# Performance work log

Hardware: AMD Instinct MI355X
Metric: run time of the kernel (lower is better)

Reference implementation:

```python
import jax, jax.numpy as jnp
import numpy as np

# ---------- constants ----------
EPS = 1e-5
_rng = np.random.default_rng(0)
_P = _rng.normal(size=(8, 3))
_P /= np.linalg.norm(_P, axis=1, keepdims=True)

def _y2_np(p):
    x, y, z = p[:, 0], p[:, 1], p[:, 2]
    return np.stack([x * y, y * z, 3 * z * z - 1, x * z, x * x - y * y], axis=-1)

_A2 = np.linalg.pinv(_y2_np(_P)).astype(np.float32)  # [5,8]
P_C = jnp.asarray(_P.astype(np.float32))
A2_C = jnp.asarray(_A2)
NORM_CONST = np.float32(1.0 / np.sqrt(20.0))  # avg_num_neighbors ** -0.5
# res update (buffer zeros, not learnable): sigmoid(0)=0.5
_U = 0.5
C_OLD = np.float32(1.0 / np.sqrt(_U * _U + 1.0))
C_NEW = np.float32(_U * C_OLD)


def _y2(p):  # real l=2 monomial basis on unit vectors
    x, y, z = p[..., 0], p[..., 1], p[..., 2]
    return jnp.stack([x * y, y * z, 3.0 * z * z - 1.0, x * z, x * x - y * y], axis=-1)


def _frame(v):  # [E,3] -> R [E,3,3] with R @ v_hat = z
    n = v / jnp.linalg.norm(v, axis=-1, keepdims=True)
    z = jnp.array([0.0, 0.0, 1.0], v.dtype)
    xa = jnp.array([1.0, 0.0, 0.0], v.dtype)
    a = jnp.where(jnp.abs(n[:, 2:3]) < 0.99, z, xa)
    e1 = jnp.cross(a, n)
    e1 = e1 / jnp.linalg.norm(e1, axis=-1, keepdims=True)
    e2 = jnp.cross(n, e1)
    return jnp.stack([e1, e2, n], axis=1)


def _wigner_d2(R):  # [E,3,3] -> D2 [E,5,5] via sample-point fit
    pts = jnp.einsum('pj,eij->epi', P_C, R)  # R @ p_k, [E,8,3]
    M = _y2(pts)  # [E,8,5] = Y_P @ D^T
    Dt = jnp.einsum('ap,epb->eab', A2_C, M)  # [E,5,5]
    return jnp.swapaxes(Dt, 1, 2)


def _sln(x, w0, b0, w1, w2):  # separable equivariant layernorm, 32x0e+16x1e+8x2e
    s = x[:, :32]
    v1 = x[:, 32:80].reshape(-1, 16, 3)
    v2 = x[:, 80:120].reshape(-1, 8, 5)
    mu = jnp.mean(s, axis=-1, keepdims=True)
    var = jnp.mean((s - mu) ** 2, axis=-1, keepdims=True)
    s = (s - mu) * jax.lax.rsqrt(var + EPS) * w0 + b0
    var1 = jnp.mean(v1 ** 2, axis=(1, 2))  # degree-balanced component variance
    var2 = jnp.mean(v2 ** 2, axis=(1, 2))
    inv = jax.lax.rsqrt(0.5 * (var1 + var2) + EPS)[:, None, None]
    v1 = v1 * inv * w1[None, :, None]
    v2 = v2 * inv * w2[None, :, None]
    return jnp.concatenate([s, v1.reshape(-1, 48), v2.reshape(-1, 40)], axis=-1)


def _ir_linear(x, W0, b0, W1, W2):  # irreps-wise linear 32x0e+16x1e+8x2e -> same
    s = x[:, :32] @ (W0 / np.sqrt(32.0)) + b0
    v1 = jnp.einsum('eui,uv->evi', x[:, 32:80].reshape(-1, 16, 3), W1) / np.sqrt(16.0)
    v2 = jnp.einsum('eui,uv->evi', x[:, 80:120].reshape(-1, 8, 5), W2) / np.sqrt(8.0)
    return jnp.concatenate([s, v1.reshape(-1, 48), v2.reshape(-1, 40)], axis=-1)


def _so2(x_cat, R, D2f, D2b, w):  # SO2 linear with per-edge dynamic weights
    E = x_cat.shape[0]
    w0 = w[:, :8960].reshape(E, 112, 80)
    w1r = w[:, 8960:10112].reshape(E, 48, 24)
    w1i = w[:, 10112:11264].reshape(E, 48, 24)
    w2r = w[:, 11264:11392].reshape(E, 16, 8)
    w2i = w[:, 11392:11520].reshape(E, 16, 8)
    # split concatenated [in + hidden] blocks
    s = jnp.concatenate([x_cat[:, :32], x_cat[:, 120:152]], axis=-1)  # [E,64]
    v1 = jnp.concatenate([x_cat[:, 32:80].reshape(E, 16, 3),
                          x_cat[:, 152:200].reshape(E, 16, 3)], axis=1)  # [E,32,3]
    v2 = jnp.concatenate([x_cat[:, 80:120].reshape(E, 8, 5),
                          x_cat[:, 200:240].reshape(E, 16 // 2, 5)], axis=1)  # [E,16,5]
    # rotate into edge-aligned frame
    v1 = jnp.einsum('eij,euj->eui', R, v1)
    v2 = jnp.einsum('eij,euj->eui', D2f, v2)
    in0 = jnp.concatenate([s, v1[:, :, 1], v2[:, :, 2]], axis=-1)   # m=0, [E,112]
    inn1 = jnp.concatenate([v1[:, :, 0], v2[:, :, 1]], axis=-1)     # m=-1, [E,48]
    inp1 = jnp.concatenate([v1[:, :, 2], v2[:, :, 3]], axis=-1)     # m=+1
    inn2 = v2[:, :, 0]  # m=-2
    inp2 = v2[:, :, 4]  # m=+2
    out0 = jnp.einsum('ei,eio->eo', in0, w0) / np.sqrt(112.0)
    op1 = (jnp.einsum('ei,eio->eo', inp1, w1r) - jnp.einsum('ei,eio->eo', inn1, w1i)) / np.sqrt(48.0)
    on1 = (jnp.einsum('ei,eio->eo', inn1, w1r) + jnp.einsum('ei,eio->eo', inp1, w1i)) / np.sqrt(48.0)
    op2 = (jnp.einsum('ei,eio->eo', inp2, w2r) - jnp.einsum('ei,eio->eo', inn2, w2i)) / np.sqrt(16.0)
    on2 = (jnp.einsum('ei,eio->eo', inn2, w2r) + jnp.einsum('ei,eio->eo', inp2, w2i)) / np.sqrt(16.0)
    s_out = out0[:, :56]
    y1 = jnp.stack([on1[:, :16], out0[:, 56:72], op1[:, :16]], axis=-1)  # [E,16,3]
    y2o = jnp.stack([on2, on1[:, 16:24], out0[:, 72:80], op1[:, 16:24], op2], axis=-1)  # [E,8,5]
    # rotate back
    y1 = jnp.einsum('eij,euj->eui', jnp.swapaxes(R, 1, 2), y1)
    y2o = jnp.einsum('eij,euj->eui', D2b, y2o)
    return jnp.concatenate([s_out, y1.reshape(E, 48), y2o.reshape(E, 40)], axis=-1)  # [E,144]


def _gate(m):  # 32x0e scalars | 24x0e gates | 16x1e+8x2e gated
    s = jax.nn.silu(m[:, :32])
    g = jax.nn.sigmoid(m[:, 32:56])
    v1 = m[:, 56:104].reshape(-1, 16, 3) * g[:, :16, None]
    v2 = m[:, 104:144].reshape(-1, 8, 5) * g[:, 16:24, None]
    return jnp.concatenate([s, v1.reshape(-1, 48), v2.reshape(-1, 40)], axis=-1)


def _env(m, we):  # E3ElementLinear: per-mul elementwise weights
    s = m[:, :32] * we[:, :32]
    v1 = m[:, 32:80].reshape(-1, 16, 3) * we[:, 32:48, None]
    v2 = m[:, 80:120].reshape(-1, 8, 5) * we[:, 48:56, None]
    return jnp.concatenate([s, v1.reshape(-1, 48), v2.reshape(-1, 40)], axis=-1)


def setup_inputs() -> dict:
    key = jax.random.key(0)
    ks = jax.random.split(key, 16)
    N, E, L = 512, 10240, 128
    inp = {
        'latents': jax.random.normal(ks[0], (E, L), jnp.float32),
        'node_features': jax.random.normal(ks[1], (N, 120), jnp.float32),
        'hidden_features': jax.random.normal(ks[2], (E, 120), jnp.float32),
        'node_onehot': jnp.ones((N, 16), jnp.float32),
        'edge_vector': jax.random.normal(ks[3], (E, 3), jnp.float32),
        'W_tp': jax.random.normal(ks[4], (L, 11520), jnp.float32),
        'W_env': jax.random.normal(ks[5], (L, 56), jnp.float32),
        'sln_w0': jnp.ones((32,), jnp.float32),
        'sln_b0': jnp.zeros((32,), jnp.float32),
        'sln_w1': jnp.ones((16,), jnp.float32),
        'sln_w2': jnp.ones((8,), jnp.float32),
        'Wp0': jax.random.normal(ks[6], (32, 32), jnp.float32),
        'bp0': jnp.zeros((32,), jnp.float32),
        'Wp1': jax.random.normal(ks[7], (16, 16), jnp.float32),
        'Wp2': jax.random.normal(ks[8], (8, 8), jnp.float32),
        'Wr0': jax.random.normal(ks[9], (32, 32), jnp.float32),
        'br0': jnp.zeros((32,), jnp.float32),
        'Wr1': jax.random.normal(ks[10], (16, 16), jnp.float32),
        'Wr2': jax.random.normal(ks[11], (8, 8), jnp.float32),
        'atom_type': jax.random.randint(ks[12], (N,), 0, 10, jnp.int32),
        'edge_index': jax.random.randint(ks[13], (2, E), 0, N, jnp.int32),
        'active_edges': jnp.arange(E, dtype=jnp.int32),
    }
    return inp


def reference(latents, node_features, hidden_features, node_onehot, edge_vector,
              W_tp, W_env, sln_w0, sln_b0, sln_w1, sln_w2,
              Wp0, bp0, Wp1, Wp2, Wr0, br0, Wr1, Wr2,
              atom_type, edge_index, active_edges):
    n_nodes = node_features.shape[0]
    center = edge_index[0][active_edges]
    nf = _sln(node_features, sln_w0, sln_b0, sln_w1, sln_w2)
    x_cat = jnp.concatenate([nf[center], hidden_features], axis=-1)  # [E,240]
    v = edge_vector[active_edges]
    R = _frame(v)
    D2f = _wigner_d2(R)
    D2b = _wigner_d2(jnp.swapaxes(R, 1, 2))
    wdyn = latents @ (W_tp / np.sqrt(128.0))  # per-edge dynamic SO2 weights
    msg = _so2(x_cat, R, D2f, D2b, wdyn)
    msg = _gate(msg)
    msg = _ir_linear(msg, Wp0, bp0, Wp1, Wp2)
    wenv = latents[active_edges] @ (W_env / np.sqrt(128.0))
    weighted = _env(msg, wenv)
    new_nf = jax.ops.segment_sum(weighted, center, num_segments=n_nodes)
    new_nf = new_nf * NORM_CONST
    res = _ir_linear(node_features, Wr0, br0, Wr1, Wr2)
    return C_NEW * new_nf + C_OLD * res
```

## Files before the change

kernel.cpp:

```cpp
#include <hip/hip_runtime.h>
#include <math.h>

#define E_TOT   10240
#define N_NODES 512
#define NCOL    11520

typedef unsigned short ushort_t;
typedef unsigned int   uint_t;
typedef __bf16 bf16x8 __attribute__((ext_vector_type(8)));
typedef float  f32x4  __attribute__((ext_vector_type(4)));

constexpr float EPSF        = 1e-5f;
constexpr float INV_SQRT128 = 0.08838834764831845f;
constexpr float INV_SQRT112 = 0.09449111825230681f;
constexpr float INV_SQRT48  = 0.14433756729740643f;
constexpr float INV_SQRT32  = 0.17677669529663687f;
constexpr float INV_SQRT16  = 0.25f;
constexpr float INV_SQRT8   = 0.35355339059327373f;
constexpr float SC0 = INV_SQRT128 * INV_SQRT112;
constexpr float SC1 = INV_SQRT128 * INV_SQRT48;
constexpr float SC2 = INV_SQRT128 * INV_SQRT16;
constexpr float C_OLD_ = 0.8944271909999159f;
constexpr float C_NEW_ = 0.4472135954999579f;
constexpr float NORMC  = 0.22360679774997896f;

__device__ __forceinline__ ushort_t f2bf(float x) {
  uint_t u = __float_as_uint(x);
  u = (u + 0x7fffu + ((u >> 16) & 1u)) >> 16;
  return (ushort_t)u;
}

__device__ __forceinline__ void wigner5(const float q[9], float D[25]) {
  const float q0x=q[0],q0y=q[1],q0z=q[2];
  const float q1x=q[3],q1y=q[4],q1z=q[5];
  const float q2x=q[6],q2y=q[7],q2z=q[8];
  D[0]  = q0x*q1y + q1x*q0y;
  D[1]  = q0y*q1z + q1y*q0z;
  D[2]  = 0.5f*(q0z*q1z);
  D[3]  = q0x*q1z + q1x*q0z;
  D[4]  = 0.5f*(q0x*q1x - q0y*q1y);
  D[5]  = q1x*q2y + q2x*q1y;
  D[6]  = q1y*q2z + q2y*q1z;
  D[7]  = 0.5f*(q1z*q2z);
  D[8]  = q1x*q2z + q2x*q1z;
  D[9]  = 0.5f*(q1x*q2x - q1y*q2y);
  D[10] = 6.f*q2x*q2y;
  D[11] = 6.f*q2y*q2z;
  D[12] = 0.5f*(3.f*q2z*q2z - 1.f);
  D[13] = 6.f*q2x*q2z;
  D[14] = 1.5f*(q2x*q2x - q2y*q2y);
  D[15] = q0x*q2y + q2x*q0y;
  D[16] = q0y*q2z + q2y*q0z;
  D[17] = 0.5f*(q0z*q2z);
  D[18] = q0x*q2z + q2x*q0z;
  D[19] = 0.5f*(q0x*q2x - q0y*q2y);
  D[20] = 2.f*(q0x*q0y - q1x*q1y);
  D[21] = 2.f*(q0y*q0z - q1y*q1z);
  D[22] = 0.5f*(q0z*q0z - q1z*q1z);
  D[23] = 2.f*(q0x*q0z - q1x*q1z);
  D[24] = 0.5f*((q0x*q0x - q1x*q1x) - (q0y*q0y - q1y*q1y));
}

__global__ void kA(const float* __restrict__ Wtp, const float* __restrict__ lat,
                   const float* __restrict__ Wenv,
                   ushort_t* __restrict__ Wp,
                   ushort_t* __restrict__ lath, ushort_t* __restrict__ latl,
                   float* __restrict__ oa_g, float* __restrict__ accg,
                   float* __restrict__ WenvT) {
  __shared__ float Wl[128*17];
  const int bid = blockIdx.x;
  const int t = threadIdx.x;
  if (bid < 720) {
    const int nt = bid;
    int col, tt;
    if (nt < 560)      { col = nt/112; tt = nt - col*112; }
    else if (nt < 608) { col = 5;  tt = nt-560; }
    else if (nt < 632) { col = 6;  tt = nt-608; }
    else if (nt < 680) { col = 7;  tt = nt-632; }
    else if (nt < 704) { col = 8;  tt = nt-680; }
    else if (nt < 712) { col = 9;  tt = nt-704; }
    else               { col = 10; tt = nt-712; }
    float sc;
    {
      const int m1 = t & 15, lp = t >> 4;
      int c;
      switch (col) {
        case 5:  c = 8960  + tt*24 + m1;                        sc = SC1; break;
        case 6:  c = 8960  + (2*tt + (m1>>3))*24 + 16 + (m1&7); sc = SC1; break;
        case 7:  c = 10112 + tt*24 + m1;                        sc = SC1; break;
        case 8:  c = 10112 + (2*tt + (m1>>3))*24 + 16 + (m1&7); sc = SC1; break;
        case 9:  c = 11264 + (2*tt + (m1>>3))*8 + (m1&7);       sc = SC2; break;
        case 10: c = 11392 + (2*tt + (m1>>3))*8 + (m1&7);       sc = SC2; break;
        default: c = tt*80 + col*16 + m1;                       sc = SC0; break;
      }
#pragma unroll
      for (int p = 0; p < 8; ++p) {
        int l = p*16 + lp;
        Wl[l*17 + m1] = Wtp[(size_t)l*NCOL + c] * sc;
      }
    }
    __syncthreads();
    const int kc = t >> 6, lane = t & 63;
    const int m = lane & 15, kg = lane >> 4;
    ushort_t hi[8], lo[8];
#pragma unroll
    for (int jj = 0; jj < 8; ++jj) {
      int l = kc*32 + kg*8 + jj;
      float w = Wl[l*17 + m];
      ushort_t h = f2bf(w);
      float hf = __uint_as_float(((uint_t)h) << 16);
      hi[jj] = h;
      lo[jj] = f2bf(w - hf);
    }
    size_t base = ((size_t)nt*8 + kc*2)*512 + (size_t)lane*8;
    *(uint4*)&Wp[base]       = *(const uint4*)hi;
    *(uint4*)&Wp[base + 512] = *(const uint4*)lo;
    return;
  }
  const int j = bid - 720;
  const int idx = j*256 + t;
  {
    float x = lat[idx];
    ushort_t h = f2bf(x);
    float hf = __uint_as_float(((uint_t)h) << 16);
    lath[idx] = h;
    latl[idx] = f2bf(x - hf);
  }
#pragma unroll
  for (int i = t; i < 288; i += 256) oa_g[(size_t)j*288 + i] = 0.f;
  if (j < 240) accg[j*256 + t] = 0.f;
  if (j >= 4000 && j < 4028) {
    int q = (j-4000)*256 + t;
    int o = q >> 7, l = q & 127;
    WenvT[o*128 + l] = Wenv[l*56 + o];
  }
}

__global__ __launch_bounds__(256)
void k2_edge_prep(const float* __restrict__ ndf,
                  const float* __restrict__ hid,
                  const float* __restrict__ evec,
                  const int*   __restrict__ eidx,
                  const int*   __restrict__ act,
                  const float* __restrict__ w0, const float* __restrict__ b0,
                  const float* __restrict__ w1, const float* __restrict__ w2,
                  float* __restrict__ invT,
                  float* __restrict__ Rm,
                  float* __restrict__ D2bm) {
  __shared__ float xs[32][240];
  __shared__ float Rs[32][9];
  __shared__ float Dfs[32][25];
  __shared__ float muS[32], isS[32], invS[32];
  __shared__ int   ctrs[32];
  const int t = threadIdx.x;
  const int e0 = blockIdx.x*32;
  if (t < 32) {
    const int e = e0 + t;
    const int ae = act[e];
    ctrs[t] = eidx[ae];
    float vx = evec[ae*3+0], vy = evec[ae*3+1], vz = evec[ae*3+2];
    float rn = rsqrtf(vx*vx + vy*vy + vz*vz);
    float nx = vx*rn, ny = vy*rn, nz = vz*rn;
    float e1x, e1y, e1z;
    if (fabsf(nz) < 0.99f) { e1x = -ny; e1y = nx;  e1z = 0.f; }
    else                   { e1x = 0.f; e1y = -nz; e1z = ny;  }
    float rl = rsqrtf(e1x*e1x + e1y*e1y + e1z*e1z);
    e1x *= rl; e1y *= rl; e1z *= rl;
    float e2x = ny*e1z - nz*e1y;
    float e2y = nz*e1x - nx*e1z;
    float e2z = nx*e1y - ny*e1x;
    float R[9] = {e1x,e1y,e1z, e2x,e2y,e2z, nx,ny,nz};
#pragma unroll
    for (int jj = 0; jj < 9; ++jj) { Rs[t][jj] = R[jj]; Rm[(size_t)e*9 + jj] = R[jj]; }
    float Df[25];
    wigner5(R, Df);
#pragma unroll
    for (int jj = 0; jj < 25; ++jj) Dfs[t][jj] = Df[jj];
    float Rt[9] = {R[0],R[3],R[6], R[1],R[4],R[7], R[2],R[5],R[8]};
    float Db[25];
    wigner5(Rt, Db);
#pragma unroll
    for (int jj = 0; jj < 25; ++jj) D2bm[(size_t)e*25 + jj] = Db[jj];
  }
  __syncthreads();
  for (int i = t; i < 32*120; i += 256) {
    int s = i/120, jj = i - s*120;
    xs[s][jj]     = ndf[(size_t)ctrs[s]*120 + jj];
    xs[s][120+jj] = hid[(size_t)(e0+s)*120 + jj];
  }
  __syncthreads();
  if (t < 32) {
    float sum = 0.f, sq = 0.f;
#pragma unroll
    for (int i = 0; i < 32; ++i) { float v = xs[t][i]; sum += v; sq += v*v; }
    float mu = sum*(1.f/32.f);
    float var = sq*(1.f/32.f) - mu*mu;
    float v1s = 0.f, v2s = 0.f;
#pragma unroll
    for (int i = 32; i < 80; ++i) { float v = xs[t][i]; v1s += v*v; }
#pragma unroll
    for (int i = 80; i < 120; ++i) { float v = xs[t][i]; v2s += v*v; }
    muS[t] = mu;
    isS[t] = rsqrtf(var + EPSF);
    invS[t] = rsqrtf(0.5f*(v1s*(1.f/48.f) + v2s*(1.f/40.f)) + EPSF);
  }
  __syncthreads();
  const int e = t & 31, rb = t >> 5;
  const float* X  = xs[e];
  const float* Rr = Rs[e];
  const float* Df = Dfs[e];
  const float mu = muS[e], istd = isS[e], inv = invS[e];
#pragma unroll
  for (int r = rb; r < 240; r += 8) {
    float val;
    if (r < 64) {
      if (r < 32) val = (X[r] - mu)*istd*w0[r] + b0[r];
      else        val = X[88 + r];
    } else if (r < 96) {
      int u = r - 64; int b; float fac;
      if (u < 16) { b = 32 + 3*u; fac = inv*w1[u]; } else { b = 152 + 3*(u-16); fac = 1.f; }
      val = (Rr[3]*X[b] + Rr[4]*X[b+1] + Rr[5]*X[b+2])*fac;
    } else if (r < 112) {
      int u = r - 96; int b; float fac;
      if (u < 8) { b = 80 + 5*u; fac = inv*w2[u]; } else { b = 200 + 5*(u-8); fac = 1.f; }
      val = (Df[10]*X[b] + Df[11]*X[b+1] + Df[12]*X[b+2] + Df[13]*X[b+3] + Df[14]*X[b+4])*fac;
    } else if (r < 160) {
      int u = r - 112;
      if (u < 32) {
        int b; float fac;
        if (u < 16) { b = 32 + 3*u; fac = inv*w1[u]; } else { b = 152 + 3*(u-16); fac = 1.f; }
        val = (Rr[0]*X[b] + Rr[1]*X[b+1] + Rr[2]*X[b+2])*fac;
      } else {
        int u2 = u - 32; int b; float fac;
        if (u2 < 8) { b = 80 + 5*u2; fac = inv*w2[u2]; } else { b = 200 + 5*(u2-8); fac = 1.f; }
        val = (Df[5]*X[b] + Df[6]*X[b+1] + Df[7]*X[b+2] + Df[8]*X[b+3] + Df[9]*X[b+4])*fac;
      }
    } else if (r < 208) {
      int u = r - 160;
      if (u < 32) {
        int b; float fac;
        if (u < 16) { b = 32 + 3*u; fac = inv*w1[u]; } else { b = 152 + 3*(u-16); fac = 1.f; }
        val = (Rr[6]*X[b] + Rr[7]*X[b+1] + Rr[8]*X[b+2])*fac;
      } else {
        int u2 = u - 32; int b; float fac;
        if (u2 < 8) { b = 80 + 5*u2; fac = inv*w2[u2]; } else { b = 200 + 5*(u2-8); fac = 1.f; }
        val = (Df[15]*X[b] + Df[16]*X[b+1] + Df[17]*X[b+2] + Df[18]*X[b+3] + Df[19]*X[b+4])*fac;
      }
    } else if (r < 224) {
      int u = r - 208; int b; float fac;
      if (u < 8) { b = 80 + 5*u; fac = inv*w2[u]; } else { b = 200 + 5*(u-8); fac = 1.f; }
      val = (Df[0]*X[b] + Df[1]*X[b+1] + Df[2]*X[b+2] + Df[3]*X[b+3] + Df[4]*X[b+4])*fac;
    } else {
      int u = r - 224; int b; float fac;
      if (u < 8) { b = 80 + 5*u; fac = inv*w2[u]; } else { b = 200 + 5*(u-8); fac = 1.f; }
      val = (Df[20]*X[b] + Df[21]*X[b+1] + Df[22]*X[b+2] + Df[23]*X[b+3] + Df[24]*X[b+4])*fac;
    }
    invT[(size_t)r*E_TOT + e0 + e] = val;
  }
}

__global__ __launch_bounds__(256, 2)
void k3_gemm(const ushort_t* __restrict__ Wp,
             const ushort_t* __restrict__ lath,
             const ushort_t* __restrict__ latl,
             const float*  __restrict__ invT,
             float* __restrict__ oa_g) {
  __shared__ __align__(16) ushort_t abuf[2][8192];
  const int t = threadIdx.x;
  const int wave = t >> 6, lane = t & 63;
  const int le = lane & 15, g = lane >> 4, gh = g >> 1;
  const int fbase = blockIdx.y * 40;
  const int e0w = blockIdx.x*128 + wave*32;
  bf16x8 Bh[4][2], Bl[4][2];
#pragma unroll
  for (int kc = 0; kc < 4; ++kc)
#pragma unroll
    for (int n = 0; n < 2; ++n) {
      size_t off = (size_t)(e0w + n*16 + le)*128 + kc*32 + g*8;
      Bh[kc][n] = *(const bf16x8*)(lath + off);
      Bl[kc][n] = *(const bf16x8*)(latl + off);
    }
  int col, tt;
  if (fbase < 560)      { col = fbase/112; tt = fbase - col*112; }
  else if (fbase < 608) { col = 5;  tt = fbase-560; }
  else if (fbase < 632) { col = 6;  tt = fbase-608; }
  else if (fbase < 680) { col = 7;  tt = fbase-632; }
  else if (fbase < 704) { col = 8;  tt = fbase-680; }
  else if (fbase < 712) { col = 9;  tt = fbase-704; }
  else                  { col = 10; tt = fbase-712; }
  int mP_, mN_, sP_, sN_, segLen; float sg_; bool PAIR_, TWO_;
  auto setParams = [&](int cf) {
    if (cf < 5)       { segLen=112; mP_=0;   mN_=0;   sP_=cf*16; sN_=0;   sg_=1.f;  PAIR_=false; TWO_=false; }
    else if (cf == 5) { segLen=48;  mP_=160; mN_=112; sP_=80;  sN_=104; sg_=1.f;  PAIR_=false; TWO_=true; }
    else if (cf == 6) { segLen=24;  mP_=160; mN_=112; sP_=96;  sN_=120; sg_=1.f;  PAIR_=true;  TWO_=true; }
    else if (cf == 7) { segLen=48;  mP_=112; mN_=160; sP_=80;  sN_=104; sg_=-1.f; PAIR_=false; TWO_=true; }
    else if (cf == 8) { segLen=24;  mP_=112; mN_=160; sP_=96;  sN_=120; sg_=-1.f; PAIR_=true;  TWO_=true; }
    else if (cf == 9) { segLen=8;   mP_=224; mN_=208; sP_=128; sN_=136; sg_=1.f;  PAIR_=true;  TWO_=true; }
    else              { segLen=8;   mP_=208; mN_=224; sP_=128; sN_=136; sg_=-1.f; PAIR_=true;  TWO_=true; }
  };
  setParams(col);
  f32x4 aP0={0,0,0,0}, aP1={0,0,0,0}, aN0={0,0,0,0}, aN1={0,0,0,0};
  auto flush = [&]() {
#pragma unroll
    for (int r = 0; r < 4; ++r) {
      int mm = g*4 + r;
      int sp = sP_ + (PAIR_ ? (mm & 7) : mm);
      atomicAdd(&oa_g[(size_t)(e0w + le)*144 + sp], sg_*aP0[r]);
      atomicAdd(&oa_g[(size_t)(e0w + 16 + le)*144 + sp], sg_*aP1[r]);
      if (TWO_) {
        int sn = sN_ + (PAIR_ ? (mm & 7) : mm);
        atomicAdd(&oa_g[(size_t)(e0w + le)*144 + sn], aN0[r]);
        atomicAdd(&oa_g[(size_t)(e0w + 16 + le)*144 + sn], aN1[r]);
      }
    }
    aP0 = (f32x4){0,0,0,0}; aP1 = (f32x4){0,0,0,0};
    aN0 = (f32x4){0,0,0,0}; aN1 = (f32x4){0,0,0,0};
  };
#pragma unroll
  for (int qq = 0; qq < 4; ++qq) {
    uint4 v = *(const uint4*)(Wp + ((size_t)fbase*8 + wave*4 + qq)*512 + lane*8);
    *(uint4*)&abuf[0][(wave*4 + qq)*512 + lane*8] = v;
  }
  __syncthreads();
  for (int c = 0; c < 20; ++c) {
    const int cb = c & 1, nb = cb ^ 1;
    uint4 pre[4];
    const bool more = (c + 1) < 20;
    if (more) {
#pragma unroll
      for (int qq = 0; qq < 4; ++qq)
        pre[qq] = *(const uint4*)(Wp + ((size_t)(fbase + 2*(c+1))*8 + wave*4 + qq)*512 + lane*8);
    }
#pragma unroll
    for (int lt = 0; lt < 2; ++lt) {
      int idx = PAIR_ ? (2*tt + gh) : tt;
      int rowP = mP_ + idx;
      float mP0 = invT[(size_t)rowP*E_TOT + e0w + le];
      float mP1 = invT[(size_t)rowP*E_TOT + e0w + 16 + le];
      float mN0 = 0.f, mN1 = 0.f;
      if (TWO_) {
        int rowN = mN_ + idx;
        mN0 = invT[(size_t)rowN*E_TOT + e0w + le];
        mN1 = invT[(size_t)rowN*E_TOT + e0w + 16 + le];
      }
      f32x4 d0 = {0,0,0,0}, d1 = {0,0,0,0};
#pragma unroll
      for (int kc = 0; kc < 4; ++kc) {
        bf16x8 Ah = *(const bf16x8*)&abuf[cb][(lt*8 + kc*2 + 0)*512 + lane*8];
        bf16x8 Al = *(const bf16x8*)&abuf[cb][(lt*8 + kc*2 + 1)*512 + lane*8];
        d0 = __builtin_amdgcn_mfma_f32_16x16x32_bf16(Ah, Bh[kc][0], d0, 0, 0, 0);
        d1 = __builtin_amdgcn_mfma_f32_16x16x32_bf16(Ah, Bh[kc][1], d1, 0, 0, 0);
        d0 = __builtin_amdgcn_mfma_f32_16x16x32_bf16(Ah, Bl[kc][0], d0, 0, 0, 0);
        d1 = __builtin_amdgcn_mfma_f32_16x16x32_bf16(Ah, Bl[kc][1], d1, 0, 0, 0);
        d0 = __builtin_amdgcn_mfma_f32_16x16x32_bf16(Al, Bh[kc][0], d0, 0, 0, 0);
        d1 = __builtin_amdgcn_mfma_f32_16x16x32_bf16(Al, Bh[kc][1], d1, 0, 0, 0);
      }
#pragma unroll
      for (int r = 0; r < 4; ++r) { aP0[r] += mP0*d0[r]; aP1[r] += mP1*d1[r]; }
      if (TWO_) {
#pragma unroll
        for (int r = 0; r < 4; ++r) { aN0[r] += mN0*d0[r]; aN1[r] += mN1*d1[r]; }
      }
      tt++;
      if (tt == segLen) { flush(); col++; tt = 0; setParams(col); }
    }
    if (more) {
#pragma unroll
      for (int qq = 0; qq < 4; ++qq)
        *(uint4*)&abuf[nb][(wave*4 + qq)*512 + lane*8] = pre[qq];
    }
    __syncthreads();
  }
  if (tt > 0) flush();
}

__global__ __launch_bounds__(256)
void k4_epi(const float* __restrict__ oa_g, const float* __restrict__ Rm,
            const float* __restrict__ D2bm,
            const float* __restrict__ lat, const float* __restrict__ WenvT,
            const int* __restrict__ eidx, const int* __restrict__ act,
            const float* __restrict__ Wp0, const float* __restrict__ bp0,
            const float* __restrict__ Wp1, const float* __restrict__ Wp2,
            float* __restrict__ accg) {
  __shared__ float sc[4][200];
  const int wave = threadIdx.x >> 6, lane = threadIdx.x & 63;
  const int eg = blockIdx.x*4 + wave;
  const int ae = act[eg];
  const float* o_ = oa_g + (size_t)eg*144;
  if (lane < 56) {
    const float4* wv = (const float4*)(WenvT + lane*128);
    const float4* lv = (const float4*)(lat + (size_t)ae*128);
    float4 s4 = {0,0,0,0};
#pragma unroll
    for (int l4 = 0; l4 < 32; ++l4) {
      float4 a = lv[l4], b = wv[l4];
      s4.x += a.x*b.x; s4.y += a.y*b.y; s4.z += a.z*b.z; s4.w += a.w*b.w;
    }
    sc[wave][144 + lane] = (s4.x + s4.y + s4.z + s4.w) * INV_SQRT128;
    float v = o_[lane];
    sc[wave][lane] = (lane < 32) ? v/(1.f + expf(-v)) : 1.f/(1.f + expf(-v));
  }
  __syncthreads();
  const float* Rr = Rm + (size_t)eg*9;
  const float* Db = D2bm + (size_t)eg*25;
  if (lane < 48) {
    int u = lane/3, cc = lane - u*3;
    float yx = o_[104+u], yy = o_[56+u], yz = o_[80+u];
    float p = Rr[cc]*yx + Rr[3+cc]*yy + Rr[6+cc]*yz;
    sc[wave][56+lane] = p * sc[wave][32+u];
  }
  __syncthreads();
  if (lane < 40) {
    int u = lane/5, ii = lane - u*5;
    float y0 = o_[136+u], y1v = o_[120+u], y2v = o_[72+u], y3 = o_[96+u], y4 = o_[128+u];
    float p = Db[ii*5+0]*y0 + Db[ii*5+1]*y1v + Db[ii*5+2]*y2v + Db[ii*5+3]*y3 + Db[ii*5+4]*y4;
    sc[wave][104+lane] = p * sc[wave][48+u];
  }
  __syncthreads();
  const int ctr = eidx[ae];
  float* dst = accg + (size_t)ctr*120;
  const float* we = &sc[wave][144];
#pragma unroll
  for (int rnd = 0; rnd < 2; ++rnd) {
    int jo = rnd*64 + lane;
    if (jo < 120) {
      float val;
      if (jo < 32) {
        float s = 0.f;
#pragma unroll
        for (int i2 = 0; i2 < 32; ++i2) s += sc[wave][i2]*Wp0[i2*32 + jo];
        val = (s*INV_SQRT32 + bp0[jo]) * we[jo];
      } else if (jo < 80) {
        int jj = jo-32, v = jj/3, cc = jj - v*3;
        float s = 0.f;
#pragma unroll
        for (int u = 0; u < 16; ++u) s += sc[wave][56 + u*3 + cc]*Wp1[u*16 + v];
        val = s*INV_SQRT16*we[32+v];
      } else {
        int jj = jo-80, v = jj/5, ii = jj - v*5;
        float s = 0.f;
#pragma unroll
        for (int u = 0; u < 8; ++u) s += sc[wave][104 + u*5 + ii]*Wp2[u*8 + v];
        val = s*INV_SQRT8*we[48+v];
      }
      atomicAdd(&dst[jo], val);
    }
  }
}

__global__ void k5_final(const float* __restrict__ x_all,
                         const float* __restrict__ Wr0, const float* __restrict__ br0,
                         const float* __restrict__ Wr1, const float* __restrict__ Wr2,
                         const float* __restrict__ accg,
                         float* __restrict__ out) {
  const int n = blockIdx.x;
  const int t = threadIdx.x;
  if (t >= 120) return;
  const float* x = x_all + n*120;
  float r;
  if (t < 32) {
    float s = 0.f;
#pragma unroll
    for (int i = 0; i < 32; ++i) s += x[i]*Wr0[i*32 + t];
    r = s*INV_SQRT32 + br0[t];
  } else if (t < 80) {
    int j = t - 32, v = j/3, cp = j - 3*v;
    float s = 0.f;
#pragma unroll
    for (int u = 0; u < 16; ++u) s += x[32 + u*3 + cp]*Wr1[u*16 + v];
    r = s*INV_SQRT16;
  } else {
    int j = t - 80, v = j/5, cp = j - 5*v;
    float s = 0.f;
#pragma unroll
    for (int u = 0; u < 8; ++u) s += x[80 + u*5 + cp]*Wr2[u*8 + v];
    r = s*INV_SQRT8;
  }
  out[n*120 + t] = C_NEW_*(NORMC*accg[n*120 + t]) + C_OLD_*r;
}

extern "C" void kernel_launch(void* const* d_in, const int* in_sizes, int n_in,
                              void* d_out, int out_size, void* d_ws, size_t ws_size,
                              hipStream_t stream) {
  const float* lat  = (const float*)d_in[0];
  const float* ndf  = (const float*)d_in[1];
  const float* hid  = (const float*)d_in[2];
  const float* evec = (const float*)d_in[4];
  const float* Wtp  = (const float*)d_in[5];
  const float* Wenv = (const float*)d_in[6];
  const float* w0   = (const float*)d_in[7];
  const float* b0   = (const float*)d_in[8];
  const float* w1   = (const float*)d_in[9];
  const float* w2   = (const float*)d_in[10];
  const float* Wp0  = (const float*)d_in[11];
  const float* bp0  = (const float*)d_in[12];
  const float* Wp1  = (const float*)d_in[13];
  const float* Wp2  = (const float*)d_in[14];
  const float* Wr0  = (const float*)d_in[15];
  const float* br0  = (const float*)d_in[16];
  const float* Wr1  = (const float*)d_in[17];
  const float* Wr2  = (const float*)d_in[18];
  const int*   eidx = (const int*)d_in[20];
  const int*   act  = (const int*)d_in[21];
  float* out = (float*)d_out;

  char* p = (char*)d_ws;
  float*    invT  = (float*)(p + 245760);
  float*    Rm    = (float*)(p + 10076160);
  float*    D2bm  = (float*)(p + 10444800);
  float*    accg  = (float*)(p + 13762560);
  float*    oa_g  = (float*)(p + 14008320);
  ushort_t* lath  = (ushort_t*)(p + 19906560);
  ushort_t* latl  = (ushort_t*)(p + 22528000);
  ushort_t* Wpack = (ushort_t*)(p + 25149440);
  float*    WenvT = (float*)(p + 31047680);

  kA<<<5840, 256, 0, stream>>>(Wtp, lat, Wenv, Wpack, lath, latl, oa_g, accg, WenvT);
  k2_edge_prep<<<E_TOT/32, 256, 0, stream>>>(ndf, hid, evec, eidx, act,
                                             w0, b0, w1, w2, invT, Rm, D2bm);
  k3_gemm<<<dim3(E_TOT/128, 18), 256, 0, stream>>>(Wpack, lath, latl, invT, oa_g);
  k4_epi<<<E_TOT/4, 256, 0, stream>>>(oa_g, Rm, D2bm, lat, WenvT, eidx, act,
                                      Wp0, bp0, Wp1, Wp2, accg);
  k5_final<<<N_NODES, 128, 0, stream>>>(ndf, Wr0, br0, Wr1, Wr2, accg, out);
}
```

Before: 324.6 us.

## Fuse prep kernels, scatter directly into output, double GEMM tile per block

Result: faster. 303.3 us (-6.5%).

```diff
diff --git a/kernel.cpp b/kernel.cpp
--- a/kernel.cpp
+++ b/kernel.cpp
@@ -23,6 +23,7 @@
 constexpr float C_OLD_ = 0.8944271909999159f;
 constexpr float C_NEW_ = 0.4472135954999579f;
 constexpr float NORMC  = 0.22360679774997896f;
+constexpr float OUTSC  = C_NEW_ * NORMC;
 
 __device__ __forceinline__ ushort_t f2bf(float x) {
   uint_t u = __float_as_uint(x);
@@ -61,16 +62,26 @@
   D[24] = 0.5f*((q0x*q0x - q1x*q1x) - (q0y*q0y - q1y*q1y));
 }
 
-__global__ void kA(const float* __restrict__ Wtp, const float* __restrict__ lat,
-                   const float* __restrict__ Wenv,
-                   ushort_t* __restrict__ Wp,
-                   ushort_t* __restrict__ lath, ushort_t* __restrict__ latl,
-                   float* __restrict__ oa_g, float* __restrict__ accg,
-                   float* __restrict__ WenvT) {
-  __shared__ float Wl[128*17];
+__global__ __launch_bounds__(256)
+void kAB(const float* __restrict__ Wtp, const float* __restrict__ lat,
+         const float* __restrict__ Wenv,
+         const float* __restrict__ ndf, const float* __restrict__ hid,
+         const float* __restrict__ evec,
+         const int* __restrict__ eidx, const int* __restrict__ act,
+         const float* __restrict__ w0, const float* __restrict__ b0,
+         const float* __restrict__ w1, const float* __restrict__ w2,
+         const float* __restrict__ Wr0, const float* __restrict__ br0,
+         const float* __restrict__ Wr1, const float* __restrict__ Wr2,
+         ushort_t* __restrict__ Wp,
+         ushort_t* __restrict__ lath, ushort_t* __restrict__ latl,
+         float* __restrict__ oa_g, float* __restrict__ WenvT,
+         float* __restrict__ invT, float* __restrict__ Rm,
+         float* __restrict__ D2bm, float* __restrict__ out) {
+  __shared__ __align__(16) char smem[35584];
   const int bid = blockIdx.x;
   const int t = threadIdx.x;
   if (bid < 720) {
+    float* Wl = (float*)smem;
     const int nt = bid;
     int col, tt;
     if (nt < 560)      { col = nt/112; tt = nt - col*112; }
@@ -80,10 +91,9 @@
     else if (nt < 704) { col = 8;  tt = nt-680; }
     else if (nt < 712) { col = 9;  tt = nt-704; }
     else               { col = 10; tt = nt-712; }
-    float sc;
     {
       const int m1 = t & 15, lp = t >> 4;
-      int c;
+      int c; float sc;
       switch (col) {
         case 5:  c = 8960  + tt*24 + m1;                        sc = SC1; break;
         case 6:  c = 8960  + (2*tt + (m1>>3))*24 + 16 + (m1&7); sc = SC1; break;
@@ -117,146 +127,179 @@
     *(uint4*)&Wp[base + 512] = *(const uint4*)lo;
     return;
   }
-  const int j = bid - 720;
-  const int idx = j*256 + t;
-  {
+  if (bid < 5840) {
+    const int j = bid - 720;
+    const int idx = j*256 + t;
     float x = lat[idx];
     ushort_t h = f2bf(x);
     float hf = __uint_as_float(((uint_t)h) << 16);
     lath[idx] = h;
     latl[idx] = f2bf(x - hf);
-  }
-#pragma unroll
-  for (int i = t; i < 288; i += 256) oa_g[(size_t)j*288 + i] = 0.f;
-  if (j < 240) accg[j*256 + t] = 0.f;
-  if (j >= 4000 && j < 4028) {
-    int q = (j-4000)*256 + t;
-    int o = q >> 7, l = q & 127;
-    WenvT[o*128 + l] = Wenv[l*56 + o];
-  }
-}
-
-__global__ __launch_bounds__(256)
-void k2_edge_prep(const float* __restrict__ ndf,
-                  const float* __restrict__ hid,
-                  const float* __restrict__ evec,
-                  const int*   __restrict__ eidx,
-                  const int*   __restrict__ act,
-                  const float* __restrict__ w0, const float* __restrict__ b0,
-                  const float* __restrict__ w1, const float* __restrict__ w2,
-                  float* __restrict__ invT,
-                  float* __restrict__ Rm,
-                  float* __restrict__ D2bm) {
-  __shared__ float xs[32][240];
-  __shared__ float Rs[32][9];
-  __shared__ float Dfs[32][25];
-  __shared__ float muS[32], isS[32], invS[32];
-  __shared__ int   ctrs[32];
-  const int t = threadIdx.x;
-  const int e0 = blockIdx.x*32;
-  if (t < 32) {
-    const int e = e0 + t;
-    const int ae = act[e];
-    ctrs[t] = eidx[ae];
-    float vx = evec[ae*3+0], vy = evec[ae*3+1], vz = evec[ae*3+2];
-    float rn = rsqrtf(vx*vx + vy*vy + vz*vz);
-    float nx = vx*rn, ny = vy*rn, nz = vz*rn;
-    float e1x, e1y, e1z;
-    if (fabsf(nz) < 0.99f) { e1x = -ny; e1y = nx;  e1z = 0.f; }
-    else                   { e1x = 0.f; e1y = -nz; e1z = ny;  }
-    float rl = rsqrtf(e1x*e1x + e1y*e1y + e1z*e1z);
-    e1x *= rl; e1y *= rl; e1z *= rl;
-    float e2x = ny*e1z - nz*e1y;
-    float e2y = nz*e1x - nx*e1z;
-    float e2z = nx*e1y - ny*e1x;
-    float R[9] = {e1x,e1y,e1z, e2x,e2y,e2z, nx,ny,nz};
-#pragma unroll
-    for (int jj = 0; jj < 9; ++jj) { Rs[t][jj] = R[jj]; Rm[(size_t)e*9 + jj] = R[jj]; }
-    float Df[25];
-    wigner5(R, Df);
-#pragma unroll
-    for (int jj = 0; jj < 25; ++jj) Dfs[t][jj] = Df[jj];
-    float Rt[9] = {R[0],R[3],R[6], R[1],R[4],R[7], R[2],R[5],R[8]};
-    float Db[25];
-    wigner5(Rt, Db);
-#pragma unroll
-    for (int jj = 0; jj < 25; ++jj) D2bm[(size_t)e*25 + jj] = Db[jj];
-  }
-  __syncthreads();
-  for (int i = t; i < 32*120; i += 256) {
-    int s = i/120, jj = i - s*120;
-    xs[s][jj]     = ndf[(size_t)ctrs[s]*120 + jj];
-    xs[s][120+jj] = hid[(size_t)(e0+s)*120 + jj];
-  }
-  __syncthreads();
-  if (t < 32) {
-    float sum = 0.f, sq = 0.f;
-#pragma unroll
-    for (int i = 0; i < 32; ++i) { float v = xs[t][i]; sum += v; sq += v*v; }
-    float mu = sum*(1.f/32.f);
-    float var = sq*(1.f/32.f) - mu*mu;
-    float v1s = 0.f, v2s = 0.f;
-#pragma unroll
-    for (int i = 32; i < 80; ++i) { float v = xs[t][i]; v1s += v*v; }
-#pragma unroll
-    for (int i = 80; i < 120; ++i) { float v = xs[t][i]; v2s += v*v; }
-    muS[t] = mu;
-    isS[t] = rsqrtf(var + EPSF);
-    invS[t] = rsqrtf(0.5f*(v1s*(1.f/48.f) + v2s*(1.f/40.f)) + EPSF);
-  }
-  __syncthreads();
-  const int e = t & 31, rb = t >> 5;
-  const float* X  = xs[e];
-  const float* Rr = Rs[e];
-  const float* Df = Dfs[e];
-  const float mu = muS[e], istd = isS[e], inv = invS[e];
-#pragma unroll
-  for (int r = rb; r < 240; r += 8) {
-    float val;
-    if (r < 64) {
-      if (r < 32) val = (X[r] - mu)*istd*w0[r] + b0[r];
-      else        val = X[88 + r];
-    } else if (r < 96) {
-      int u = r - 64; int b; float fac;
-      if (u < 16) { b = 32 + 3*u; fac = inv*w1[u]; } else { b = 152 + 3*(u-16); fac = 1.f; }
-      val = (Rr[3]*X[b] + Rr[4]*X[b+1] + Rr[5]*X[b+2])*fac;
-    } else if (r < 112) {
-      int u = r - 96; int b; float fac;
-      if (u < 8) { b = 80 + 5*u; fac = inv*w2[u]; } else { b = 200 + 5*(u-8); fac = 1.f; }
-      val = (Df[10]*X[b] + Df[11]*X[b+1] + Df[12]*X[b+2] + Df[13]*X[b+3] + Df[14]*X[b+4])*fac;
-    } else if (r < 160) {
-      int u = r - 112;
-      if (u < 32) {
-        int b; float fac;
+#pragma unroll
+    for (int i = t; i < 288; i += 256) oa_g[(size_t)j*288 + i] = 0.f;
+    if (j >= 4000 && j < 4028) {
+      int q = (j-4000)*256 + t;
+      int o = q >> 7, l = q & 127;
+      WenvT[o*128 + l] = Wenv[l*56 + o];
+    }
+    return;
+  }
+  if (bid < 6160) {
+    float (*xs)[240] = (float(*)[240])smem;
+    float (*Rs)[9]   = (float(*)[9])(smem + 30720);
+    float (*Dfs)[25] = (float(*)[25])(smem + 31872);
+    float* muS  = (float*)(smem + 35072);
+    float* isS  = (float*)(smem + 35200);
+    float* invS = (float*)(smem + 35328);
+    int*   ctrs = (int*)(smem + 35456);
+    const int e0 = (bid - 5840)*32;
+    if (t < 32) {
+      const int e = e0 + t;
+      const int ae = act[e];
+      ctrs[t] = eidx[ae];
+      float vx = evec[ae*3+0], vy = evec[ae*3+1], vz = evec[ae*3+2];
+      float rn = rsqrtf(vx*vx + vy*vy + vz*vz);
+      float nx = vx*rn, ny = vy*rn, nz = vz*rn;
+      float e1x, e1y, e1z;
+      if (fabsf(nz) < 0.99f) { e1x = -ny; e1y = nx;  e1z = 0.f; }
+      else                   { e1x = 0.f; e1y = -nz; e1z = ny;  }
+      float rl = rsqrtf(e1x*e1x + e1y*e1y + e1z*e1z);
+      e1x *= rl; e1y *= rl; e1z *= rl;
+      float e2x = ny*e1z - nz*e1y;
+      float e2y = nz*e1x - nx*e1z;
+      float e2z = nx*e1y - ny*e1x;
+      float R[9] = {e1x,e1y,e1z, e2x,e2y,e2z, nx,ny,nz};
+#pragma unroll
+      for (int jj = 0; jj < 9; ++jj) { Rs[t][jj] = R[jj]; Rm[(size_t)e*9 + jj] = R[jj]; }
+      float Df[25];
+      wigner5(R, Df);
+#pragma unroll
+      for (int jj = 0; jj < 25; ++jj) Dfs[t][jj] = Df[jj];
+      float Rt[9] = {R[0],R[3],R[6], R[1],R[4],R[7], R[2],R[5],R[8]};
+      float Db[25];
+      wigner5(Rt, Db);
+#pragma unroll
+      for (int jj = 0; jj < 25; ++jj) D2bm[(size_t)e*25 + jj] = Db[jj];
+    }
+    __syncthreads();
+    for (int i = t; i < 32*120; i += 256) {
+      int s = i/120, jj = i - s*120;
+      xs[s][jj]     = ndf[(size_t)ctrs[s]*120 + jj];
+      xs[s][120+jj] = hid[(size_t)(e0+s)*120 + jj];
+    }
+    __syncthreads();
+    if (t < 32) {
+      float sum = 0.f, sq = 0.f;
+#pragma unroll
+      for (int i = 0; i < 32; ++i) { float v = xs[t][i]; sum += v; sq += v*v; }
+      float mu = sum*(1.f/32.f);
+      float var = sq*(1.f/32.f) - mu*mu;
+      float v1s = 0.f, v2s = 0.f;
+#pragma unroll
+      for (int i = 32; i < 80; ++i) { float v = xs[t][i]; v1s += v*v; }
+#pragma unroll
+      for (int i = 80; i < 120; ++i) { float v = xs[t][i]; v2s += v*v; }
+      muS[t] = mu;
+      isS[t] = rsqrtf(var + EPSF);
+      invS[t] = rsqrtf(0.5f*(v1s*(1.f/48.f) + v2s*(1.f/40.f)) + EPSF);
+    }
+    __syncthreads();
+    const int e = t & 31, rb = t >> 5;
+    const float* X  = xs[e];
+    const float* Rr = Rs[e];
+    const float* Df = Dfs[e];
+    const float mu = muS[e], istd = isS[e], inv = invS[e];
+#pragma unroll
+    for (int r = rb; r < 240; r += 8) {
+      float val;
+      if (r < 64) {
+        if (r < 32) val = (X[r] - mu)*istd*w0[r] + b0[r];
+        else        val = X[88 + r];
+      } else if (r < 96) {
+        int u = r - 64; int b; float fac;
         if (u < 16) { b = 32 + 3*u; fac = inv*w1[u]; } else { b = 152 + 3*(u-16); fac = 1.f; }
-        val = (Rr[0]*X[b] + Rr[1]*X[b+1] + Rr[2]*X[b+2])*fac;
+        val = (Rr[3]*X[b] + Rr[4]*X[b+1] + Rr[5]*X[b+2])*fac;
+      } else if (r < 112) {
+        int u = r - 96; int b; float fac;
+        if (u < 8) { b = 80 + 5*u; fac = inv*w2[u]; } else { b = 200 + 5*(u-8); fac = 1.f; }
+        val = (Df[10]*X[b] + Df[11]*X[b+1] + Df[12]*X[b+2] + Df[13]*X[b+3] + Df[14]*X[b+4])*fac;
+      } else if (r < 160) {
+        int u = r - 112;
+        if (u < 32) {
+          int b; float fac;
+          if (u < 16) { b = 32 + 3*u; fac = inv*w1[u]; } else { b = 152 + 3*(u-16); fac = 1.f; }
+          val = (Rr[0]*X[b] + Rr[1]*X[b+1] + Rr[2]*X[b+2])*fac;
+        } else {
+          int u2 = u - 32; int b; float fac;
+          if (u2 < 8) { b = 80 + 5*u2; fac = inv*w2[u2]; } else { b = 200 + 5*(u2-8); fac = 1.f; }
+          val = (Df[5]*X[b] + Df[6]*X[b+1] + Df[7]*X[b+2] + Df[8]*X[b+3] + Df[9]*X[b+4])*fac;
+        }
+      } else if (r < 208) {
+        int u = r - 160;
+        if (u < 32) {
+          int b; float fac;
+          if (u < 16) { b = 32 + 3*u; fac = inv*w1[u]; } else { b = 152 + 3*(u-16); fac = 1.f; }
+          val = (Rr[6]*X[b] + Rr[7]*X[b+1] + Rr[8]*X[b+2])*fac;
+        } else {
+          int u2 = u - 32; int b; float fac;
+          if (u2 < 8) { b = 80 + 5*u2; fac = inv*w2[u2]; } else { b = 200 + 5*(u2-8); fac = 1.f; }
+          val = (Df[15]*X[b] + Df[16]*X[b+1] + Df[17]*X[b+2] + Df[18]*X[b+3] + Df[19]*X[b+4])*fac;
+        }
+      } else if (r < 224) {
+        int u = r - 208; int b; float fac;
+        if (u < 8) { b = 80 + 5*u; fac = inv*w2[u]; } else { b = 200 + 5*(u-8); fac = 1.f; }
+        val = (Df[0]*X[b] + Df[1]*X[b+1] + Df[2]*X[b+2] + Df[3]*X[b+3] + Df[4]*X[b+4])*fac;
       } else {
-        int u2 = u - 32; int b; float fac;
-        if (u2 < 8) { b = 80 + 5*u2; fac = inv*w2[u2]; } else { b = 200 + 5*(u2-8); fac = 1.f; }
-        val = (Df[5]*X[b] + Df[6]*X[b+1] + Df[7]*X[b+2] + Df[8]*X[b+3] + Df[9]*X[b+4])*fac;
-      }
-    } else if (r < 208) {
-      int u = r - 160;
-      if (u < 32) {
-        int b; float fac;
-        if (u < 16) { b = 32 + 3*u; fac = inv*w1[u]; } else { b = 152 + 3*(u-16); fac = 1.f; }
-        val = (Rr[6]*X[b] + Rr[7]*X[b+1] + Rr[8]*X[b+2])*fac;
-      } else {
-        int u2 = u - 32; int b; float fac;
-        if (u2 < 8) { b = 80 + 5*u2; fac = inv*w2[u2]; } else { b = 200 + 5*(u2-8); fac = 1.f; }
-        val = (Df[15]*X[b] + Df[16]*X[b+1] + Df[17]*X[b+2] + Df[18]*X[b+3] + Df[19]*X[b+4])*fac;
-      }
-    } else if (r < 224) {
-      int u = r - 208; int b; float fac;
-      if (u < 8) { b = 80 + 5*u; fac = inv*w2[u]; } else { b = 200 + 5*(u-8); fac = 1.f; }
-      val = (Df[0]*X[b] + Df[1]*X[b+1] + Df[2]*X[b+2] + Df[3]*X[b+3] + Df[4]*X[b+4])*fac;
+        int u = r - 224; int b; float fac;
+        if (u < 8) { b = 80 + 5*u; fac = inv*w2[u]; } else { b = 200 + 5*(u-8); fac = 1.f; }
+        val = (Df[20]*X[b] + Df[21]*X[b+1] + Df[22]*X[b+2] + Df[23]*X[b+3] + Df[24]*X[b+4])*fac;
+      }
+      invT[(size_t)r*E_TOT + e0 + e] = val;
+    }
+    return;
+  }
+  {
+    const int n = bid - 6160;
+    if (t >= 120) return;
+    const float* x = ndf + (size_t)n*120;
+    float r;
+    if (t < 32) {
+      float s = 0.f;
+#pragma unroll
+      for (int i = 0; i < 32; ++i) s += x[i]*Wr0[i*32 + t];
+      r = s*INV_SQRT32 + br0[t];
+    } else if (t < 80) {
+      int j = t - 32, v = j/3, cp = j - 3*v;
+      float s = 0.f;
+#pragma unroll
+      for (int u = 0; u < 16; ++u) s += x[32 + u*3 + cp]*Wr1[u*16 + v];
+      r = s*INV_SQRT16;
     } else {
-      int u = r - 224; int b; float fac;
-      if (u < 8) { b = 80 + 5*u; fac = inv*w2[u]; } else { b = 200 + 5*(u-8); fac = 1.f; }
-      val = (Df[20]*X[b] + Df[21]*X[b+1] + Df[22]*X[b+2] + Df[23]*X[b+3] + Df[24]*X[b+4])*fac;
-    }
-    invT[(size_t)r*E_TOT + e0 + e] = val;
-  }
+      int j = t - 80, v = j/5, cp = j - 5*v;
+      float s = 0.f;
+#pragma unroll
+      for (int u = 0; u < 8; ++u) s += x[80 + u*5 + cp]*Wr2[u*8 + v];
+      r = s*INV_SQRT8;
+    }
+    out[(size_t)n*120 + t] = C_OLD_*r;
+  }
+}
+
+struct Seg { int col, tt, mP, mN, sP, sN, segLen; float sg; bool PAIR, TWO; };
+__device__ __forceinline__ void setp(Seg& s) {
+  const int cf = s.col;
+  if (cf < 5)       { s.segLen=112; s.mP=0;   s.mN=0;   s.sP=cf*16; s.sN=0;   s.sg=1.f;  s.PAIR=false; s.TWO=false; }
+  else if (cf == 5) { s.segLen=48;  s.mP=160; s.mN=112; s.sP=80;  s.sN=104; s.sg=1.f;  s.PAIR=false; s.TWO=true; }
+  else if (cf == 6) { s.segLen=24;  s.mP=160; s.mN=112; s.sP=96;  s.sN=120; s.sg=1.f;  s.PAIR=true;  s.TWO=true; }
+  else if (cf == 7) { s.segLen=48;  s.mP=112; s.mN=160; s.sP=80;  s.sN=104; s.sg=-1.f; s.PAIR=false; s.TWO=true; }
+  else if (cf == 8) { s.segLen=24;  s.mP=112; s.mN=160; s.sP=96;  s.sN=120; s.sg=-1.f; s.PAIR=true;  s.TWO=true; }
+  else if (cf == 9) { s.segLen=8;   s.mP=224; s.mN=208; s.sP=128; s.sN=136; s.sg=1.f;  s.PAIR=true;  s.TWO=true; }
+  else              { s.segLen=8;   s.mP=208; s.mN=224; s.sP=128; s.sN=136; s.sg=-1.f; s.PAIR=true;  s.TWO=true; }
+}
+__device__ __forceinline__ bool adv(Seg& s) {
+  s.tt++;
+  if (s.tt == s.segLen) { s.col++; s.tt = 0; setp(s); return true; }
+  return false;
 }
 
 __global__ __launch_bounds__(256, 2)
@@ -269,7 +312,7 @@
   const int t = threadIdx.x;
   const int wave = t >> 6, lane = t & 63;
   const int le = lane & 15, g = lane >> 4, gh = g >> 1;
-  const int fbase = blockIdx.y * 40;
+  const int fbase = blockIdx.y * 80;
   const int e0w = blockIdx.x*128 + wave*32;
   bf16x8 Bh[4][2], Bl[4][2];
 #pragma unroll
@@ -280,35 +323,25 @@
       Bh[kc][n] = *(const bf16x8*)(lath + off);
       Bl[kc][n] = *(const bf16x8*)(latl + off);
     }
-  int col, tt;
-  if (fbase < 560)      { col = fbase/112; tt = fbase - col*112; }
-  else if (fbase < 608) { col = 5;  tt = fbase-560; }
-  else if (fbase < 632) { col = 6;  tt = fbase-608; }
-  else if (fbase < 680) { col = 7;  tt = fbase-632; }
-  else if (fbase < 704) { col = 8;  tt = fbase-680; }
-  else if (fbase < 712) { col = 9;  tt = fbase-704; }
-  else                  { col = 10; tt = fbase-712; }
-  int mP_, mN_, sP_, sN_, segLen; float sg_; bool PAIR_, TWO_;
-  auto setParams = [&](int cf) {
-    if (cf < 5)       { segLen=112; mP_=0;   mN_=0;   sP_=cf*16; sN_=0;   sg_=1.f;  PAIR_=false; TWO_=false; }
-    else if (cf == 5) { segLen=48;  mP_=160; mN_=112; sP_=80;  sN_=104; sg_=1.f;  PAIR_=false; TWO_=true; }
-    else if (cf == 6) { segLen=24;  mP_=160; mN_=112; sP_=96;  sN_=120; sg_=1.f;  PAIR_=true;  TWO_=true; }
-    else if (cf == 7) { segLen=48;  mP_=112; mN_=160; sP_=80;  sN_=104; sg_=-1.f; PAIR_=false; TWO_=true; }
-    else if (cf == 8) { segLen=24;  mP_=112; mN_=160; sP_=96;  sN_=120; sg_=-1.f; PAIR_=true;  TWO_=true; }
-    else if (cf == 9) { segLen=8;   mP_=224; mN_=208; sP_=128; sN_=136; sg_=1.f;  PAIR_=true;  TWO_=true; }
-    else              { segLen=8;   mP_=208; mN_=224; sP_=128; sN_=136; sg_=-1.f; PAIR_=true;  TWO_=true; }
-  };
-  setParams(col);
+  Seg s;
+  if (fbase < 560)      { s.col = fbase/112; s.tt = fbase - s.col*112; }
+  else if (fbase < 608) { s.col = 5;  s.tt = fbase-560; }
+  else if (fbase < 632) { s.col = 6;  s.tt = fbase-608; }
+  else if (fbase < 680) { s.col = 7;  s.tt = fbase-632; }
+  else if (fbase < 704) { s.col = 8;  s.tt = fbase-680; }
+  else if (fbase < 712) { s.col = 9;  s.tt = fbase-704; }
+  else                  { s.col = 10; s.tt = fbase-712; }
+  setp(s);
   f32x4 aP0={0,0,0,0}, aP1={0,0,0,0}, aN0={0,0,0,0}, aN1={0,0,0,0};
-  auto flush = [&]() {
+  auto flushSeg = [&](const Seg& fs) {
 #pragma unroll
     for (int r = 0; r < 4; ++r) {
       int mm = g*4 + r;
-      int sp = sP_ + (PAIR_ ? (mm & 7) : mm);
-      atomicAdd(&oa_g[(size_t)(e0w + le)*144 + sp], sg_*aP0[r]);
-      atomicAdd(&oa_g[(size_t)(e0w + 16 + le)*144 + sp], sg_*aP1[r]);
-      if (TWO_) {
-        int sn = sN_ + (PAIR_ ? (mm & 7) : mm);
+      int sp = fs.sP + (fs.PAIR ? (mm & 7) : mm);
+      atomicAdd(&oa_g[(size_t)(e0w + le)*144 + sp], fs.sg*aP0[r]);
+      atomicAdd(&oa_g[(size_t)(e0w + 16 + le)*144 + sp], fs.sg*aP1[r]);
+      if (fs.TWO) {
+        int sn = fs.sN + (fs.PAIR ? (mm & 7) : mm);
         atomicAdd(&oa_g[(size_t)(e0w + le)*144 + sn], aN0[r]);
         atomicAdd(&oa_g[(size_t)(e0w + 16 + le)*144 + sn], aN1[r]);
       }
@@ -322,47 +355,102 @@
     *(uint4*)&abuf[0][(wave*4 + qq)*512 + lane*8] = v;
   }
   __syncthreads();
-  for (int c = 0; c < 20; ++c) {
+  for (int c = 0; c < 40; ++c) {
     const int cb = c & 1, nb = cb ^ 1;
     uint4 pre[4];
-    const bool more = (c + 1) < 20;
+    const bool more = (c + 1) < 40;
     if (more) {
 #pragma unroll
       for (int qq = 0; qq < 4; ++qq)
         pre[qq] = *(const uint4*)(Wp + ((size_t)(fbase + 2*(c+1))*8 + wave*4 + qq)*512 + lane*8);
     }
-#pragma unroll
-    for (int lt = 0; lt < 2; ++lt) {
-      int idx = PAIR_ ? (2*tt + gh) : tt;
-      int rowP = mP_ + idx;
-      float mP0 = invT[(size_t)rowP*E_TOT + e0w + le];
-      float mP1 = invT[(size_t)rowP*E_TOT + e0w + 16 + le];
-      float mN0 = 0.f, mN1 = 0.f;
-      if (TWO_) {
-        int rowN = mN_ + idx;
-        mN0 = invT[(size_t)rowN*E_TOT + e0w + le];
-        mN1 = invT[(size_t)rowN*E_TOT + e0w + 16 + le];
-      }
-      f32x4 d0 = {0,0,0,0}, d1 = {0,0,0,0};
-#pragma unroll
-      for (int kc = 0; kc < 4; ++kc) {
-        bf16x8 Ah = *(const bf16x8*)&abuf[cb][(lt*8 + kc*2 + 0)*512 + lane*8];
-        bf16x8 Al = *(const bf16x8*)&abuf[cb][(lt*8 + kc*2 + 1)*512 + lane*8];
-        d0 = __builtin_amdgcn_mfma_f32_16x16x32_bf16(Ah, Bh[kc][0], d0, 0, 0, 0);
-        d1 = __builtin_amdgcn_mfma_f32_16x16x32_bf16(Ah, Bh[kc][1], d1, 0, 0, 0);
-        d0 = __builtin_amdgcn_mfma_f32_16x16x32_bf16(Ah, Bl[kc][0], d0, 0, 0, 0);
-        d1 = __builtin_amdgcn_mfma_f32_16x16x32_bf16(Ah, Bl[kc][1], d1, 0, 0, 0);
-        d0 = __builtin_amdgcn_mfma_f32_16x16x32_bf16(Al, Bh[kc][0], d0, 0, 0, 0);
-        d1 = __builtin_amdgcn_mfma_f32_16x16x32_bf16(Al, Bh[kc][1], d1, 0, 0, 0);
-      }
-#pragma unroll
-      for (int r = 0; r < 4; ++r) { aP0[r] += mP0*d0[r]; aP1[r] += mP1*d1[r]; }
-      if (TWO_) {
-#pragma unroll
-        for (int r = 0; r < 4; ++r) { aN0[r] += mN0*d0[r]; aN1[r] += mN1*d1[r]; }
-      }
-      tt++;
-      if (tt == segLen) { flush(); col++; tt = 0; setParams(col); }
+    Seg s1 = s;
+    const bool cross0 = adv(s1);
+    const int idx0 = s.PAIR  ? (2*s.tt  + gh) : s.tt;
+    const int idx1 = s1.PAIR ? (2*s1.tt + gh) : s1.tt;
+    float g0P0 = invT[(size_t)(s.mP + idx0)*E_TOT + e0w + le];
+    float g0P1 = invT[(size_t)(s.mP + idx0)*E_TOT + e0w + 16 + le];
+    float g1P0 = invT[(size_t)(s1.mP + idx1)*E_TOT + e0w + le];
+    float g1P1 = invT[(size_t)(s1.mP + idx1)*E_TOT + e0w + 16 + le];
+    float g0N0 = 0.f, g0N1 = 0.f, g1N0 = 0.f, g1N1 = 0.f;
+    if (s.TWO) {
+      g0N0 = invT[(size_t)(s.mN + idx0)*E_TOT + e0w + le];
+      g0N1 = invT[(size_t)(s.mN + idx0)*E_TOT + e0w + 16 + le];
+    }
+    if (s1.TWO) {
+      g1N0 = invT[(size_t)(s1.mN + idx1)*E_TOT + e0w + le];
+      g1N1 = invT[(size_t)(s1.mN + idx1)*E_TOT + e0w + 16 + le];
+    }
+    {
+      f32x4 dE0={0,0,0,0}, dO0={0,0,0,0}, dE1={0,0,0,0}, dO1={0,0,0,0};
+#pragma unroll
+      for (int kc = 0; kc < 2; ++kc) {
+        bf16x8 Ah = *(const bf16x8*)&abuf[cb][(kc*2 + 0)*512 + lane*8];
+        bf16x8 Al = *(const bf16x8*)&abuf[cb][(kc*2 + 1)*512 + lane*8];
+        dE0 = __builtin_amdgcn_mfma_f32_16x16x32_bf16(Ah, Bh[kc][0], dE0, 0, 0, 0);
+        dE1 = __builtin_amdgcn_mfma_f32_16x16x32_bf16(Ah, Bh[kc][1], dE1, 0, 0, 0);
+        dE0 = __builtin_amdgcn_mfma_f32_16x16x32_bf16(Ah, Bl[kc][0], dE0, 0, 0, 0);
+        dE1 = __builtin_amdgcn_mfma_f32_16x16x32_bf16(Ah, Bl[kc][1], dE1, 0, 0, 0);
+        dE0 = __builtin_amdgcn_mfma_f32_16x16x32_bf16(Al, Bh[kc][0], dE0, 0, 0, 0);
+        dE1 = __builtin_amdgcn_mfma_f32_16x16x32_bf16(Al, Bh[kc][1], dE1, 0, 0, 0);
+      }
+#pragma unroll
+      for (int kc = 2; kc < 4; ++kc) {
+        bf16x8 Ah = *(const bf16x8*)&abuf[cb][(kc*2 + 0)*512 + lane*8];
+        bf16x8 Al = *(const bf16x8*)&abuf[cb][(kc*2 + 1)*512 + lane*8];
+        dO0 = __builtin_amdgcn_mfma_f32_16x16x32_bf16(Ah, Bh[kc][0], dO0, 0, 0, 0);
+        dO1 = __builtin_amdgcn_mfma_f32_16x16x32_bf16(Ah, Bh[kc][1], dO1, 0, 0, 0);
+        dO0 = __builtin_amdgcn_mfma_f32_16x16x32_bf16(Ah, Bl[kc][0], dO0, 0, 0, 0);
+        dO1 = __builtin_amdgcn_mfma_f32_16x16x32_bf16(Ah, Bl[kc][1], dO1, 0, 0, 0);
+        dO0 = __builtin_amdgcn_mfma_f32_16x16x32_bf16(Al, Bh[kc][0], dO0, 0, 0, 0);
+        dO1 = __builtin_amdgcn_mfma_f32_16x16x32_bf16(Al, Bh[kc][1], dO1, 0, 0, 0);
+      }
+      f32x4 d0 = dE0 + dO0, d1 = dE1 + dO1;
+#pragma unroll
+      for (int r = 0; r < 4; ++r) { aP0[r] += g0P0*d0[r]; aP1[r] += g0P1*d1[r]; }
+      if (s.TWO) {
+#pragma unroll
+        for (int r = 0; r < 4; ++r) { aN0[r] += g0N0*d0[r]; aN1[r] += g0N1*d1[r]; }
+      }
+    }
+    if (cross0) flushSeg(s);
+    {
+      f32x4 dE0={0,0,0,0}, dO0={0,0,0,0}, dE1={0,0,0,0}, dO1={0,0,0,0};
+#pragma unroll
+      for (int kc = 0; kc < 2; ++kc) {
+        bf16x8 Ah = *(const bf16x8*)&abuf[cb][(8 + kc*2 + 0)*512 + lane*8];
+        bf16x8 Al = *(const bf16x8*)&abuf[cb][(8 + kc*2 + 1)*512 + lane*8];
+        dE0 = __builtin_amdgcn_mfma_f32_16x16x32_bf16(Ah, Bh[kc][0], dE0, 0, 0, 0);
+        dE1 = __builtin_amdgcn_mfma_f32_16x16x32_bf16(Ah, Bh[kc][1], dE1, 0, 0, 0);
+        dE0 = __builtin_amdgcn_mfma_f32_16x16x32_bf16(Ah, Bl[kc][0], dE0, 0, 0, 0);
+        dE1 = __builtin_amdgcn_mfma_f32_16x16x32_bf16(Ah, Bl[kc][1], dE1, 0, 0, 0);
+        dE0 = __builtin_amdgcn_mfma_f32_16x16x32_bf16(Al, Bh[kc][0], dE0, 0, 0, 0);
+        dE1 = __builtin_amdgcn_mfma_f32_16x16x32_bf16(Al, Bh[kc][1], dE1, 0, 0, 0);
+      }
+#pragma unroll
+      for (int kc = 2; kc < 4; ++kc) {
+        bf16x8 Ah = *(const bf16x8*)&abuf[cb][(8 + kc*2 + 0)*512 + lane*8];
+        bf16x8 Al = *(const bf16x8*)&abuf[cb][(8 + kc*2 + 1)*512 + lane*8];
+        dO0 = __builtin_amdgcn_mfma_f32_16x16x32_bf16(Ah, Bh[kc][0], dO0, 0, 0, 0);
+        dO1 = __builtin_amdgcn_mfma_f32_16x16x32_bf16(Ah, Bh[kc][1], dO1, 0, 0, 0);
+        dO0 = __builtin_amdgcn_mfma_f32_16x16x32_bf16(Ah, Bl[kc][0], dO0, 0, 0, 0);
+        dO1 = __builtin_amdgcn_mfma_f32_16x16x32_bf16(Ah, Bl[kc][1], dO1, 0, 0, 0);
+        dO0 = __builtin_amdgcn_mfma_f32_16x16x32_bf16(Al, Bh[kc][0], dO0, 0, 0, 0);
+        dO1 = __builtin_amdgcn_mfma_f32_16x16x32_bf16(Al, Bh[kc][1], dO1, 0, 0, 0);
+      }
+      f32x4 d0 = dE0 + dO0, d1 = dE1 + dO1;
+#pragma unroll
+      for (int r = 0; r < 4; ++r) { aP0[r] += g1P0*d0[r]; aP1[r] += g1P1*d1[r]; }
+      if (s1.TWO) {
+#pragma unroll
+        for (int r = 0; r < 4; ++r) { aN0[r] += g1N0*d0[r]; aN1[r] += g1N1*d1[r]; }
+      }
+    }
+    {
+      Seg s2 = s1;
+      const bool cross1 = adv(s2);
+      if (cross1) flushSeg(s1);
+      s = s2;
     }
     if (more) {
 #pragma unroll
@@ -371,7 +459,7 @@
     }
     __syncthreads();
   }
-  if (tt > 0) flush();
+  if (s.tt > 0) flushSeg(s);
 }
 
 __global__ __launch_bounds__(256)
@@ -381,7 +469,7 @@
             const int* __restrict__ eidx, const int* __restrict__ act,
             const float* __restrict__ Wp0, const float* __restrict__ bp0,
             const float* __restrict__ Wp1, const float* __restrict__ Wp2,
-            float* __restrict__ accg) {
+            float* __restrict__ out) {
   __shared__ float sc[4][200];
   const int wave = threadIdx.x >> 6, lane = threadIdx.x & 63;
   const int eg = blockIdx.x*4 + wave;
@@ -418,7 +506,7 @@
   }
   __syncthreads();
   const int ctr = eidx[ae];
-  float* dst = accg + (size_t)ctr*120;
+  float* dst = out + (size_t)ctr*120;
   const float* we = &sc[wave][144];
 #pragma unroll
   for (int rnd = 0; rnd < 2; ++rnd) {
@@ -443,40 +531,9 @@
         for (int u = 0; u < 8; ++u) s += sc[wave][104 + u*5 + ii]*Wp2[u*8 + v];
         val = s*INV_SQRT8*we[48+v];
       }
-      atomicAdd(&dst[jo], val);
-    }
-  }
-}
-
-__global__ void k5_final(const float* __restrict__ x_all,
-                         const float* __restrict__ Wr0, const float* __restrict__ br0,
-                         const float* __restrict__ Wr1, const float* __restrict__ Wr2,
-                         const float* __restrict__ accg,
-                         float* __restrict__ out) {
-  const int n = blockIdx.x;
-  const int t = threadIdx.x;
-  if (t >= 120) return;
-  const float* x = x_all + n*120;
-  float r;
-  if (t < 32) {
-    float s = 0.f;
-#pragma unroll
-    for (int i = 0; i < 32; ++i) s += x[i]*Wr0[i*32 + t];
-    r = s*INV_SQRT32 + br0[t];
-  } else if (t < 80) {
-    int j = t - 32, v = j/3, cp = j - 3*v;
-    float s = 0.f;
-#pragma unroll
-    for (int u = 0; u < 16; ++u) s += x[32 + u*3 + cp]*Wr1[u*16 + v];
-    r = s*INV_SQRT16;
-  } else {
-    int j = t - 80, v = j/5, cp = j - 5*v;
-    float s = 0.f;
-#pragma unroll
-    for (int u = 0; u < 8; ++u) s += x[80 + u*5 + cp]*Wr2[u*8 + v];
-    r = s*INV_SQRT8;
-  }
-  out[n*120 + t] = C_NEW_*(NORMC*accg[n*120 + t]) + C_OLD_*r;
+      atomicAdd(&dst[jo], OUTSC*val);
+    }
+  }
 }
 
 extern "C" void kernel_launch(void* const* d_in, const int* in_sizes, int n_in,
@@ -508,18 +565,16 @@
   float*    invT  = (float*)(p + 245760);
   float*    Rm    = (float*)(p + 10076160);
   float*    D2bm  = (float*)(p + 10444800);
-  float*    accg  = (float*)(p + 13762560);
   float*    oa_g  = (float*)(p + 14008320);
   ushort_t* lath  = (ushort_t*)(p + 19906560);
   ushort_t* latl  = (ushort_t*)(p + 22528000);
   ushort_t* Wpack = (ushort_t*)(p + 25149440);
   float*    WenvT = (float*)(p + 31047680);
 
-  kA<<<5840, 256, 0, stream>>>(Wtp, lat, Wenv, Wpack, lath, latl, oa_g, accg, WenvT);
-  k2_edge_prep<<<E_TOT/32, 256, 0, stream>>>(ndf, hid, evec, eidx, act,
-                                             w0, b0, w1, w2, invT, Rm, D2bm);
-  k3_gemm<<<dim3(E_TOT/128, 18), 256, 0, stream>>>(Wpack, lath, latl, invT, oa_g);
+  kAB<<<6672, 256, 0, stream>>>(Wtp, lat, Wenv, ndf, hid, evec, eidx, act,
+                                w0, b0, w1, w2, Wr0, br0, Wr1, Wr2,
+                                Wpack, lath, latl, oa_g, WenvT, invT, Rm, D2bm, out);
+  k3_gemm<<<dim3(E_TOT/128, 9), 256, 0, stream>>>(Wpack, lath, latl, invT, oa_g);
   k4_epi<<<E_TOT/4, 256, 0, stream>>>(oa_g, Rm, D2bm, lat, WenvT, eidx, act,
-                                      Wp0, bp0, Wp1, Wp2, accg);
-  k5_final<<<N_NODES, 128, 0, stream>>>(ndf, Wr0, br0, Wr1, Wr2, accg, out);
-}
+                                      Wp0, bp0, Wp1, Wp2, out);
+}
```
